# Kernel tuning notes

Measured on AMD Instinct MI355X. Metric: run time of the kernel, lower is better.

The kernel has to match this reference:

```python
import jax, jax.numpy as jnp
import numpy as np

B, T, D, H = 2, 2048, 1024, 16
DH = D // H
PD = 6
SCALE = DH ** -0.5
_PAIRS4 = [(0, 1), (0, 2), (0, 3), (1, 2), (1, 3), (2, 3)]
_J6 = jnp.array([[0, 0, 0, 0, 0, 1], [0, 0, 0, 0, -1, 0], [0, 0, 0, 1, 0, 0],
                 [0, 0, 1, 0, 0, 0], [0, -1, 0, 0, 0, 0], [1, 0, 0, 0, 0, 0]], dtype=jnp.float32)


def exterior(p1, p2):
    # p1, p2: (..., 4) -> normalized 6-d Plucker line (..., 6)
    parts = [p1[..., i] * p2[..., j] - p1[..., j] * p2[..., i] for i, j in _PAIRS4]
    L = jnp.stack(parts, axis=-1)
    n = jnp.linalg.norm(L, axis=-1, keepdims=True)
    return L / jnp.clip(n, 1e-12)


def setup_inputs() -> dict:
    key = jax.random.key(0)
    ks = jax.random.split(key, 12)
    s = 0.02
    return {
        'x': jax.random.normal(ks[0], (B, T, D), jnp.float32),
        'qkv_w': jax.random.normal(ks[1], (D, 3 * D), jnp.float32) * s,
        'qkv_b': jnp.zeros((3 * D,), jnp.float32),
        'w1_write': jax.random.normal(ks[2], (D, 4 * H), jnp.float32) * s,
        'w2_write': jax.random.normal(ks[3], (D, 4 * H), jnp.float32) * s,
        'w1_read': jax.random.normal(ks[4], (D, 4 * H), jnp.float32) * s,
        'w2_read': jax.random.normal(ks[5], (D, 4 * H), jnp.float32) * s,
        'memv_w': jax.random.normal(ks[6], (D, D), jnp.float32) * s,
        'memv_b': jnp.zeros((D,), jnp.float32),
        'memg_w': jax.random.normal(ks[7], (D, H), jnp.float32) * s,
        'memg_b': jnp.zeros((H,), jnp.float32),
        'mem_scale': jnp.full((H,), 0.1, jnp.float32),
        'rw_mix': jnp.zeros((), jnp.float32),
        'out_w': jax.random.normal(ks[8], (D, D), jnp.float32) * s,
        'out_b': jnp.zeros((D,), jnp.float32),
        'decay_logits': jnp.full((H,), 4.6, jnp.float32),
    }


def reference(x, qkv_w, qkv_b, w1_write, w2_write, w1_read, w2_read,
              memv_w, memv_b, memg_w, memg_b, mem_scale, rw_mix,
              out_w, out_b, decay_logits):
    # ---- standard causal softmax attention ----
    qkv = (x @ qkv_w + qkv_b).reshape(B, T, 3, H, DH).transpose(2, 0, 3, 1, 4)
    q, k, v = qkv[0], qkv[1], qkv[2]                      # each (B,H,T,DH)
    scores = jnp.einsum('bhtd,bhsd->bhts', q, k) * SCALE
    mask = jnp.triu(jnp.ones((T, T), bool), 1)
    scores = jnp.where(mask[None, None], -jnp.inf, scores)
    attn = jax.nn.softmax(scores, axis=-1)                # dropout=0 (eval)
    seq_out = jnp.einsum('bhts,bhsd->bthd', attn, v).reshape(B, T, D)

    # ---- Plucker lines for write (prev->cur) and read ----
    x_prev = jnp.concatenate([jnp.zeros((B, 1, D), x.dtype), x[:, :-1]], axis=1)
    w1 = (x_prev @ w1_write).reshape(B, T, H, 4)
    w2 = (x @ w2_write).reshape(B, T, H, 4)
    write_lines = exterior(w1, w2)                        # (B,T,H,6)
    r1 = (x @ w1_read).reshape(B, T, H, 4)
    r2 = (x @ w2_read).reshape(B, T, H, 4)
    read_lines = exterior(r1, r2)

    Jw = jnp.einsum('bthi,ij->bhtj', write_lines, _J6)    # (B,H,T,6)
    Jr = jnp.einsum('bthi,ij->bhtj', read_lines, _J6)
    rd = read_lines.transpose(0, 2, 1, 3)                 # (B,H,T,6)

    # ---- decay-weighted cumsum of 6x6 outer-product states ----
    decays = jax.nn.sigmoid(decay_logits)                 # (H,)
    pos = jnp.arange(T, dtype=x.dtype)
    decay_inv = (1.0 / jnp.clip(decays, 1e-6))[:, None] ** pos[None]   # (H,T)
    decay_fwd = decays[:, None] ** pos[None]                           # (H,T)

    def shifted_state(Jv):
        outer = Jv[..., :, None] * Jv[..., None, :]       # (B,H,T,6,6)
        ow = outer * decay_inv[None, :, :, None, None]
        M = jnp.cumsum(ow, axis=2)
        M = jnp.concatenate([jnp.zeros((B, H, 1, PD, PD), x.dtype), M[:, :, :-1]], axis=2)
        return M * decay_fwd[None, :, :, None, None]

    Mw = shifted_state(Jw)
    Mr = shifted_state(Jr)

    score_w = jnp.einsum('bhti,bhtij,bhtj->bht', rd, Mw, rd)
    score_r = jnp.einsum('bhti,bhtij,bhtj->bht', Jw, Mr, Jw)
    alpha = jax.nn.sigmoid(rw_mix)
    mem_score = (1 - alpha) * score_w + alpha * score_r   # (B,H,T)

    mem_val = x @ memv_w + memv_b                         # (B,T,D)
    gate = jax.nn.sigmoid(x @ memg_w + memg_b)            # (B,T,H)
    mem_score_t = mem_score.transpose(0, 2, 1)            # (B,T,H)
    gated = jax.nn.sigmoid(mem_score_t * mem_scale[None, None, :]) * gate
    gated = gated.mean(axis=-1, keepdims=True)            # (B,T,1)

    return (seq_out + gated * mem_val) @ out_w + out_b
```

## Files before the change

kernel.cpp:

```cpp
#include <hip/hip_runtime.h>

#define Bb 2
#define Tt 2048
#define Dd 1024
#define Hh 16
#define LDC 4480

typedef __attribute__((ext_vector_type(8))) short s16x8;
typedef __attribute__((ext_vector_type(4))) float f32x4;
typedef __attribute__((ext_vector_type(8))) _Float16 f16x8;

__device__ __forceinline__ float bf2f(unsigned short u) {
  unsigned v = ((unsigned)u) << 16;
  union { unsigned u; float f; } c; c.u = v; return c.f;
}
__device__ __forceinline__ unsigned short f2bf(float f) {
  union { float f; unsigned u; } c; c.f = f;
  unsigned u = c.u + 0x7fffu + ((c.u >> 16) & 1u);
  return (unsigned short)(u >> 16);
}
__device__ __forceinline__ float sigm(float x) { return 1.f / (1.f + expf(-x)); }

__device__ __forceinline__ int swz(int row, int k) {
  return (k & ~31) | (k & 7) | (((((k >> 3) & 3) ^ ((row >> 1) & 3))) << 3);
}

__device__ __forceinline__ void async_copy16(void* lds, const void* g) {
  __builtin_amdgcn_global_load_lds(
      (const __attribute__((address_space(1))) unsigned int*)g,
      (__attribute__((address_space(3))) unsigned int*)lds, 16, 0, 0);
}


__global__ __launch_bounds__(256) void prep_kernel(const float* __restrict__ x,
                                                   const float* __restrict__ qkv_w,
                                                   const float* __restrict__ w1w,
                                                   const float* __restrict__ w2w,
                                                   const float* __restrict__ w1r,
                                                   const float* __restrict__ w2r,
                                                   const float* __restrict__ memg_w,
                                                   const float* __restrict__ memv_w,
                                                   const float* __restrict__ out_w,
                                                   const float* __restrict__ qkv_b,
                                                   const float* __restrict__ memg_b,
                                                   const float* __restrict__ memv_b,
                                                   unsigned short* __restrict__ xb,
                                                   unsigned short* __restrict__ WT,
                                                   unsigned short* __restrict__ outT,
                                                   float* __restrict__ biasC) {
  __shared__ float tile[32][33];
  int id = blockIdx.x;
  if (id < 2048) {
    int i = id * 256 + threadIdx.x;
    int row = i >> 7;
    int colbase = (i & 127) * 8;
    const float4* xv = reinterpret_cast<const float4*>(x + (size_t)i * 8);
    float4 a = xv[0], b = xv[1];
    s16x8 out;
    out[0] = (short)f2bf(a.x); out[1] = (short)f2bf(a.y);
    out[2] = (short)f2bf(a.z); out[3] = (short)f2bf(a.w);
    out[4] = (short)f2bf(b.x); out[5] = (short)f2bf(b.y);
    out[6] = (short)f2bf(b.z); out[7] = (short)f2bf(b.w);
    *(s16x8*)&xb[(size_t)row * 1024 + swz(row, colbase)] = out;
  } else if (id < 6528) {
    int j = id - 2048;
    int n0 = (j % 140) * 32, k0 = (j / 140) * 32;
    int tx = threadIdx.x & 31, ty = threadIdx.x >> 5;
#pragma unroll
    for (int i = 0; i < 4; i++) {
      int k = k0 + ty + i * 8, n = n0 + tx;
      float v;
      if (n < 3072)       v = qkv_w[(size_t)k * 3072 + n];
      else if (n < 3136)  v = w1w[k * 64 + (n - 3072)];
      else if (n < 3200)  v = w2w[k * 64 + (n - 3136)];
      else if (n < 3264)  v = w1r[k * 64 + (n - 3200)];
      else if (n < 3328)  v = w2r[k * 64 + (n - 3264)];
      else if (n < 3344)  v = memg_w[k * 16 + (n - 3328)];
      else if (n < 3392)  v = 0.f;
      else if (n < 4416)  v = memv_w[(size_t)k * 1024 + (n - 3392)];
      else                v = 0.f;
      tile[ty + i * 8][tx] = v;
    }
    __syncthreads();
#pragma unroll
    for (int i = 0; i < 4; i++) {
      int n = n0 + ty + i * 8, k = k0 + tx;
      WT[(size_t)n * 1024 + swz(n, k)] = f2bf(tile[tx][ty + i * 8]);
    }
  } else if (id < 7552) {
    int j = id - 6528;
    int n0 = (j & 31) * 32, k0 = (j >> 5) * 32;
    int tx = threadIdx.x & 31, ty = threadIdx.x >> 5;
#pragma unroll
    for (int i = 0; i < 4; i++) {
      int k = k0 + ty + i * 8, n = n0 + tx;
      tile[ty + i * 8][tx] = out_w[(size_t)k * 1024 + n];
    }
    __syncthreads();
#pragma unroll
    for (int i = 0; i < 4; i++) {
      int n = n0 + ty + i * 8, k = k0 + tx;
      outT[(size_t)n * 1024 + swz(n, k)] = f2bf(tile[tx][ty + i * 8]);
    }
  } else {
    int i = (id - 7552) * 256 + threadIdx.x;
    if (i < LDC) {
      float v = 0.f;
      if (i < 3072) v = qkv_b[i];
      else if (i >= 3328 && i < 3344) v = memg_b[i - 3328];
      else if (i >= 3392 && i < 4416) v = memv_b[i - 3392];
      biasC[i] = v;
    }
  }
}


__global__ __launch_bounds__(256) void gemm_kernel(const unsigned short* __restrict__ A,
                                                   const unsigned short* __restrict__ Bt,
                                                   unsigned short* __restrict__ Cout,
                                                   const float* __restrict__ bias) {
  const int K = 1024;
  const int x = blockIdx.x & 7, local = blockIdx.x >> 3;
  const int mTile = (x >> 1) * 8 + (local & 7);
  const int nTile = (x & 1) * 18 + (local >> 3);
  if (nTile >= 35) return;
  const int mBase = mTile * 128, nBase = nTile * 128;

  __shared__ unsigned short As0[128 * 32], As1[128 * 32];
  __shared__ unsigned short Bs0[128 * 32], Bs1[128 * 32];
  const int tid = threadIdx.x;
  const int lane = tid & 63, wid = tid >> 6;
  const int quad = lane >> 4, c16 = lane & 15;
  const int wm = wid >> 1, wn = wid & 1;
  const int srow = lane >> 2, scol = (lane & 3) << 3;
  const int slot = (quad ^ ((c16 >> 1) & 3)) * 8;

  f32x4 acc[4][4] = {};
  for (int k0 = 0; k0 < K; k0 += 64) {
    __syncthreads();
#pragma unroll
    for (int j = 0; j < 2; j++) {
      int rr = wid * 32 + j * 16;
      size_t ga = (size_t)(mBase + rr + srow) * K + k0 + scol;
      size_t gb = (size_t)(nBase + rr + srow) * K + k0 + scol;
      async_copy16(&As0[rr * 32], &A[ga]);
      async_copy16(&Bs0[rr * 32], &Bt[gb]);
      async_copy16(&As1[rr * 32], &A[ga + 32]);
      async_copy16(&Bs1[rr * 32], &Bt[gb + 32]);
    }
    __syncthreads();
#pragma unroll
    for (int kk = 0; kk < 2; kk++) {
      const unsigned short* Asp = kk ? As1 : As0;
      const unsigned short* Bsp = kk ? Bs1 : Bs0;
      s16x8 af[4], bf[4];
#pragma unroll
      for (int mt = 0; mt < 4; mt++)
        af[mt] = *(const s16x8*)&Asp[(wm * 64 + mt * 16 + c16) * 32 + slot];
#pragma unroll
      for (int nt = 0; nt < 4; nt++)
        bf[nt] = *(const s16x8*)&Bsp[(wn * 64 + nt * 16 + c16) * 32 + slot];
#pragma unroll
      for (int mt = 0; mt < 4; mt++)
#pragma unroll
        for (int nt = 0; nt < 4; nt++)
          acc[mt][nt] = __builtin_amdgcn_mfma_f32_16x16x32_bf16(af[mt], bf[nt], acc[mt][nt], 0, 0, 0);
    }
  }
#pragma unroll
  for (int mt = 0; mt < 4; mt++)
#pragma unroll
    for (int nt = 0; nt < 4; nt++) {
      int col = nBase + wn * 64 + nt * 16 + c16;
      float bv = bias[col];
#pragma unroll
      for (int r = 0; r < 4; r++) {
        int row = mBase + wm * 64 + mt * 16 + quad * 4 + r;
        Cout[(size_t)row * 4480 + col] = f2bf(acc[mt][nt][r] + bv);
      }
    }
}


__global__ __launch_bounds__(256) void gemm_out_kernel(const unsigned short* __restrict__ A,
                                                       const unsigned short* __restrict__ Bt,
                                                       float* __restrict__ Cout,
                                                       const float* __restrict__ bias) {
  const int K = 1024;
  const int mBase = blockIdx.y * 64, nBase = blockIdx.x * 128;
  __shared__ unsigned short As0[64 * 32], As1[64 * 32];
  __shared__ unsigned short Bs0[128 * 32], Bs1[128 * 32];
  const int tid = threadIdx.x;
  const int lane = tid & 63, wid = tid >> 6;
  const int quad = lane >> 4, c16 = lane & 15;
  const int wm = wid >> 1, wn = wid & 1;
  const int srow = lane >> 2, scol = (lane & 3) << 3;
  const int slot = (quad ^ ((c16 >> 1) & 3)) * 8;

  f32x4 acc[2][4] = {};
  for (int k0 = 0; k0 < K; k0 += 64) {
    __syncthreads();
    {
      int rrA = wid * 16;
      size_t ga = (size_t)(mBase + rrA + srow) * K + k0 + scol;
      async_copy16(&As0[rrA * 32], &A[ga]);
      async_copy16(&As1[rrA * 32], &A[ga + 32]);
#pragma unroll
      for (int j = 0; j < 2; j++) {
        int rr = wid * 32 + j * 16;
        size_t gb = (size_t)(nBase + rr + srow) * K + k0 + scol;
        async_copy16(&Bs0[rr * 32], &Bt[gb]);
        async_copy16(&Bs1[rr * 32], &Bt[gb + 32]);
      }
    }
    __syncthreads();
#pragma unroll
    for (int kk = 0; kk < 2; kk++) {
      const unsigned short* Asp = kk ? As1 : As0;
      const unsigned short* Bsp = kk ? Bs1 : Bs0;
      s16x8 af[2], bf[4];
#pragma unroll
      for (int mt = 0; mt < 2; mt++)
        af[mt] = *(const s16x8*)&Asp[(wm * 32 + mt * 16 + c16) * 32 + slot];
#pragma unroll
      for (int nt = 0; nt < 4; nt++)
        bf[nt] = *(const s16x8*)&Bsp[(wn * 64 + nt * 16 + c16) * 32 + slot];
#pragma unroll
      for (int mt = 0; mt < 2; mt++)
#pragma unroll
        for (int nt = 0; nt < 4; nt++)
          acc[mt][nt] = __builtin_amdgcn_mfma_f32_16x16x32_bf16(af[mt], bf[nt], acc[mt][nt], 0, 0, 0);
    }
  }
#pragma unroll
  for (int mt = 0; mt < 2; mt++)
#pragma unroll
    for (int nt = 0; nt < 4; nt++) {
      int col = nBase + wn * 64 + nt * 16 + c16;
      float bv = bias[col];
#pragma unroll
      for (int r = 0; r < 4; r++) {
        int row = mBase + wm * 32 + mt * 16 + quad * 4 + r;
        Cout[(size_t)row * 1024 + col] = acc[mt][nt][r] + bv;
      }
    }
}


__device__ __forceinline__ void ext6(const float* p, const float* q, float* L) {
  L[0] = p[0] * q[1] - p[1] * q[0];
  L[1] = p[0] * q[2] - p[2] * q[0];
  L[2] = p[0] * q[3] - p[3] * q[0];
  L[3] = p[1] * q[2] - p[2] * q[1];
  L[4] = p[1] * q[3] - p[3] * q[1];
  L[5] = p[2] * q[3] - p[3] * q[2];
  float n = sqrtf(L[0]*L[0] + L[1]*L[1] + L[2]*L[2] + L[3]*L[3] + L[4]*L[4] + L[5]*L[5]);
  float inv = 1.f / fmaxf(n, 1e-12f);
#pragma unroll
  for (int k = 0; k < 6; k++) L[k] *= inv;
}


__global__ __launch_bounds__(256) void post1_kernel(const unsigned short* __restrict__ Cq,
                                                    unsigned short* __restrict__ Kt,
                                                    unsigned short* __restrict__ Vt,
                                                    float* __restrict__ Jw,
                                                    float* __restrict__ Jr,
                                                    float* __restrict__ rd) {
  __shared__ unsigned short vt[32 * 66];
  int id = blockIdx.x;
  int tid = threadIdx.x;
  if (id < 2048) {
    int kb = id & 63, bh = id >> 6;
    int b = bh >> 4, h = bh & 15;
    size_t tbase = ((size_t)bh * 64 + kb) * 2048;
    {
      int key = tid >> 3, p = tid & 7, dg = p ^ (key & 7);
      size_t src = (size_t)(b * Tt + kb * 32 + key) * LDC + 1024 + h * 64 + dg * 8;
      s16x8 kv = *(const s16x8*)&Cq[src];
      *(s16x8*)&Kt[tbase + (size_t)tid * 8] = kv;
    }
    {
      int row = tid >> 3, c = tid & 7;
      size_t src = (size_t)(b * Tt + kb * 32 + row) * LDC + 2048 + h * 64 + c * 8;
      s16x8 vv = *(const s16x8*)&Cq[src];
#pragma unroll
      for (int e = 0; e < 8; e++) {
        union { _Float16 hf; unsigned short s; } cv;
        cv.hf = (_Float16)bf2f((unsigned short)vv[e]);
        vt[row * 66 + c * 8 + e] = cv.s;
      }
    }
    __syncthreads();
    {
      int d = tid >> 2, p = tid & 3, cq = p ^ ((d >> 2) & 3);
      s16x8 out;
#pragma unroll
      for (int e = 0; e < 8; e++) {
        int key = ((e >> 2) & 1) * 16 + cq * 4 + (e & 3);
        out[e] = (short)vt[key * 66 + d];
      }
      *(s16x8*)&Vt[tbase + (size_t)tid * 8] = out;
    }
  } else {
    int idx = (id - 2048) * 256 + tid;
    int h = idx & 15, t = (idx >> 4) & 2047, b = idx >> 15;
    size_t row = (size_t)(b * Tt + t) * LDC;
    float w1[4], w2[4], r1[4], r2[4];
#pragma unroll
    for (int k = 0; k < 4; k++) {
      w1[k] = (t > 0) ? bf2f(Cq[row - LDC + 3072 + h * 4 + k]) : 0.f;
      w2[k] = bf2f(Cq[row + 3136 + h * 4 + k]);
      r1[k] = bf2f(Cq[row + 3200 + h * 4 + k]);
      r2[k] = bf2f(Cq[row + 3264 + h * 4 + k]);
    }
    float Lw[6], Lr[6];
    ext6(w1, w2, Lw);
    ext6(r1, r2, Lr);
    size_t ob = ((size_t)(b * Hh + h) * Tt + t) * 6;
    Jw[ob + 0] = Lw[5]; Jw[ob + 1] = -Lw[4]; Jw[ob + 2] = Lw[3];
    Jw[ob + 3] = Lw[2]; Jw[ob + 4] = -Lw[1]; Jw[ob + 5] = Lw[0];
    Jr[ob + 0] = Lr[5]; Jr[ob + 1] = -Lr[4]; Jr[ob + 2] = Lr[3];
    Jr[ob + 3] = Lr[2]; Jr[ob + 4] = -Lr[1]; Jr[ob + 5] = Lr[0];
#pragma unroll
    for (int k = 0; k < 6; k++) rd[ob + k] = Lr[k];
  }
}


__device__ __forceinline__ void do_tile(int ks, int q0, int quad, int c16,
                                        const s16x8& qf0, const s16x8& qf1,
                                        const s16x8 kf[2][2], const f16x8 vb[4],
                                        float& l_i, f32x4 o[4]) {
  f32x4 st0 = {}, st1 = {};
  st0 = __builtin_amdgcn_mfma_f32_16x16x32_bf16(kf[0][0], qf0, st0, 0, 0, 0);
  st0 = __builtin_amdgcn_mfma_f32_16x16x32_bf16(kf[0][1], qf1, st0, 0, 0, 0);
  st1 = __builtin_amdgcn_mfma_f32_16x16x32_bf16(kf[1][0], qf0, st1, 0, 0, 0);
  st1 = __builtin_amdgcn_mfma_f32_16x16x32_bf16(kf[1][1], qf1, st1, 0, 0, 0);
  bool need_mask = (ks + 31 > q0);
  f16x8 pa;
  float lp = 0.f;
#pragma unroll
  for (int r = 0; r < 4; r++) {
    float v0 = st0[r] * 0.125f;
    float v1 = st1[r] * 0.125f;
    if (need_mask) {
      v0 = (ks + quad * 4 + r      <= q0 + c16) ? v0 : -1e30f;
      v1 = (ks + 16 + quad * 4 + r <= q0 + c16) ? v1 : -1e30f;
    }
    float p0 = __expf(v0);
    float p1 = __expf(v1);
    lp += p0 + p1;
    pa[r]     = (_Float16)p0;
    pa[4 + r] = (_Float16)p1;
  }
  l_i += lp;
#pragma unroll
  for (int nt = 0; nt < 4; nt++)
    o[nt] = __builtin_amdgcn_mfma_f32_16x16x32_f16(pa, vb[nt], o[nt], 0, 0, 0);
}

__global__ __launch_bounds__(256) void attn_kernel(const unsigned short* __restrict__ Cq,
                                                   const unsigned short* __restrict__ Kt,
                                                   const unsigned short* __restrict__ Vt,
                                                   unsigned short* __restrict__ po) {
  __shared__ unsigned short Kl[2048];
  __shared__ unsigned short Vl[2048];
  const int g0 = blockIdx.x, bh = blockIdx.y;
  const int g = ((bh >> 4) & 1) ? (15 - g0) : g0;
  const int b = bh >> 4, h = bh & 15;
  const int w = threadIdx.x >> 6, lane = threadIdx.x & 63;
  const int quad = lane >> 4, c16 = lane & 15;
  const int pi = g * 4 + w;
  const int qA = pi * 16, qB = 2032 - pi * 16;
  const int nkA = qA + 16, nkB = 2048 - pi * 16;
  const int bound = 2048 - 64 * g;
  const unsigned short* Ktb = Kt + (size_t)bh * 64 * 2048;
  const unsigned short* Vtb = Vt + (size_t)bh * 64 * 2048;
  const int ci = threadIdx.x;

  size_t rowA = (size_t)(b * Tt + qA + c16) * LDC + h * 64;
  size_t rowB = (size_t)(b * Tt + qB + c16) * LDC + h * 64;
  s16x8 qA0 = *(const s16x8*)&Cq[rowA + quad * 8];
  s16x8 qA1 = *(const s16x8*)&Cq[rowA + 32 + quad * 8];
  s16x8 qB0 = *(const s16x8*)&Cq[rowB + quad * 8];
  s16x8 qB1 = *(const s16x8*)&Cq[rowB + 32 + quad * 8];

  float lA = 0.f, lB = 0.f;
  f32x4 oA[4] = {}, oB[4] = {};

  {
    s16x8 k0 = *(const s16x8*)&Ktb[(size_t)ci * 8];
    s16x8 v0 = *(const s16x8*)&Vtb[(size_t)ci * 8];
    *(s16x8*)&Kl[ci * 8] = k0;
    *(s16x8*)&Vl[ci * 8] = v0;
  }
  __syncthreads();

  for (int ks = 0; ks < bound; ks += 32) {
    bool more = (ks + 32) < bound;
    s16x8 kreg, vreg;
    if (more) {
      size_t nb = ((size_t)(ks >> 5) + 1) * 2048 + (size_t)ci * 8;
      kreg = *(const s16x8*)&Ktb[nb];
      vreg = *(const s16x8*)&Vtb[nb];
    }
    if (ks < nkB) {
      s16x8 kf[2][2];
#pragma unroll
      for (int gg = 0; gg < 2; gg++)
#pragma unroll
        for (int half = 0; half < 2; half++) {
          int key = gg * 16 + c16;
          int p = (half * 4 + quad) ^ (c16 & 7);
          kf[gg][half] = *(const s16x8*)&Kl[(key * 8 + p) * 8];
        }
      f16x8 vb[4];
#pragma unroll
      for (int nt = 0; nt < 4; nt++) {
        int d = nt * 16 + c16;
        int p = quad ^ ((d >> 2) & 3);
        vb[nt] = *(const f16x8*)&Vl[(d * 4 + p) * 8];
      }
      do_tile(ks, qB, quad, c16, qB0, qB1, kf, vb, lB, oB);
      if (ks < nkA)
        do_tile(ks, qA, quad, c16, qA0, qA1, kf, vb, lA, oA);
    }
    __syncthreads();
    if (more) {
      *(s16x8*)&Kl[ci * 8] = kreg;
      *(s16x8*)&Vl[ci * 8] = vreg;
      __syncthreads();
    }
  }

  lB += __shfl_xor(lB, 16, 64); lB += __shfl_xor(lB, 32, 64);
  lA += __shfl_xor(lA, 16, 64); lA += __shfl_xor(lA, 32, 64);
  float invB = 1.f / lB, invA = 1.f / lA;
#pragma unroll
  for (int r = 0; r < 4; r++) {
    float ivB = __shfl(invB, quad * 4 + r, 64);
    float ivA = __shfl(invA, quad * 4 + r, 64);
    size_t baseB = (size_t)(b * Tt + qB + quad * 4 + r) * Dd + h * 64;
    size_t baseA = (size_t)(b * Tt + qA + quad * 4 + r) * Dd + h * 64;
#pragma unroll
    for (int nt = 0; nt < 4; nt++) {
      po[baseB + nt * 16 + c16] = f2bf(oB[nt][r] * ivB);
      po[baseA + nt * 16 + c16] = f2bf(oA[nt][r] * ivA);
    }
  }
}


__global__ __launch_bounds__(64) void scanA_kernel(const float* __restrict__ Jw,
                                                   const float* __restrict__ Jr,
                                                   const float* __restrict__ decay_logits,
                                                   float* __restrict__ chunkA) {
  int blk = blockIdx.x;
  int chunk = blk & 15, bh = (blk >> 4) & 31, type = blk >> 9;
  int lane = threadIdx.x;
  const float* V = (type == 0 ? Jw : Jr) + ((size_t)bh * Tt + chunk * 128) * 6;
  __shared__ float v[768];
  for (int i = lane; i < 768; i += 64) v[i] = V[i];
  __syncthreads();
  float d = sigm(decay_logits[bh & 15]);
  int ll = lane < 36 ? lane : 35;
  int i6 = ll / 6, j6 = ll % 6;
  float A = 0.f;
  for (int s = 0; s < 128; s++) A = d * A + v[s * 6 + i6] * v[s * 6 + j6];
  if (lane < 36) chunkA[((size_t)(type * 32 + bh) * 16 + chunk) * 36 + lane] = A;
}


__global__ __launch_bounds__(128) void scanB_kernel(const float* __restrict__ Jw,
                                                    const float* __restrict__ Jr,
                                                    const float* __restrict__ rd,
                                                    const float* __restrict__ chunkA,
                                                    const float* __restrict__ decay_logits,
                                                    float* __restrict__ score_w,
                                                    float* __restrict__ score_r) {
  int blk = blockIdx.x;
  int chunk = blk & 15, bh = (blk >> 4) & 31, type = blk >> 9;
  int tl = threadIdx.x;
  size_t tb = ((size_t)bh * Tt + chunk * 128) * 6;
  const float* U = (type == 0 ? rd : Jw) + tb;
  const float* W = (type == 0 ? Jw : Jr) + tb;
  __shared__ float wv[768];
  __shared__ float Bm[36];
  for (int i = tl; i < 768; i += 128) wv[i] = W[i];
  float d = sigm(decay_logits[bh & 15]);
  if (tl < 36) {
    float dS = powf(d, 128.f);
    float Bv = 0.f;
    size_t base = (size_t)(type * 32 + bh) * 16;
    for (int c = 0; c < chunk; c++)
      Bv = dS * Bv + d * chunkA[(base + c) * 36 + tl];
    Bm[tl] = Bv;
  }
  __syncthreads();
  float u[6];
#pragma unroll
  for (int i = 0; i < 6; i++) u[i] = U[tl * 6 + i];
  float q = 0.f;
#pragma unroll
  for (int i = 0; i < 6; i++) {
    float bi = 0.f;
#pragma unroll
    for (int j = 0; j < 6; j++) bi += Bm[i * 6 + j] * u[j];
    q += u[i] * bi;
  }
  float acc = 0.f;
  for (int s = 0; s < tl; s++) {
    const float* ws = &wv[s * 6];
    float dot = u[0]*ws[0] + u[1]*ws[1] + u[2]*ws[2] + u[3]*ws[3] + u[4]*ws[4] + u[5]*ws[5];
    acc = d * (acc + dot * dot);
  }
  float score = acc + powf(d, (float)tl) * q;
  float* outp = (type == 0 ? score_w : score_r);
  outp[(size_t)bh * Tt + chunk * 128 + tl] = score;
}


__global__ __launch_bounds__(256) void combine_kernel(const unsigned short* __restrict__ po,
                                                      const unsigned short* __restrict__ Cq,
                                                      const float* __restrict__ score_w,
                                                      const float* __restrict__ score_r,
                                                      const float* __restrict__ mem_scale,
                                                      const float* __restrict__ rw_mix,
                                                      unsigned short* __restrict__ fused) {
  __shared__ float tmp[16];
  int rowi = blockIdx.x;
  int b = rowi >> 11, t = rowi & 2047;
  float alpha = sigm(rw_mix[0]);
  if (threadIdx.x < 16) {
    int h = threadIdx.x;
    size_t sh = (size_t)(b * 16 + h) * Tt + t;
    float ms = (1.f - alpha) * score_w[sh] + alpha * score_r[sh];
    float gate = sigm(bf2f(Cq[(size_t)rowi * LDC + 3328 + h]));
    tmp[h] = sigm(ms * mem_scale[h]) * gate;
  }
  __syncthreads();
  float g = 0.f;
#pragma unroll
  for (int h = 0; h < 16; h++) g += tmp[h];
  g *= (1.f / 16.f);
  for (int d = threadIdx.x; d < Dd; d += 256) {
    float sv = bf2f(po[((size_t)b * Tt + t) * Dd + d]);
    float mv = bf2f(Cq[(size_t)rowi * LDC + 3392 + d]);
    fused[(size_t)rowi * Dd + swz(rowi, d)] = f2bf(sv + g * mv);
  }
}


extern "C" void kernel_launch(void* const* d_in, const int* in_sizes, int n_in,
                              void* d_out, int out_size, void* d_ws, size_t ws_size,
                              hipStream_t stream) {
  (void)in_sizes; (void)n_in; (void)out_size; (void)ws_size;
  const float* x         = (const float*)d_in[0];
  const float* qkv_w     = (const float*)d_in[1];
  const float* qkv_b     = (const float*)d_in[2];
  const float* w1w       = (const float*)d_in[3];
  const float* w2w       = (const float*)d_in[4];
  const float* w1r       = (const float*)d_in[5];
  const float* w2r       = (const float*)d_in[6];
  const float* memv_w    = (const float*)d_in[7];
  const float* memv_b    = (const float*)d_in[8];
  const float* memg_w    = (const float*)d_in[9];
  const float* memg_b    = (const float*)d_in[10];
  const float* mem_scale = (const float*)d_in[11];
  const float* rw_mix    = (const float*)d_in[12];
  const float* out_w     = (const float*)d_in[13];
  const float* out_b     = (const float*)d_in[14];
  const float* decay_l   = (const float*)d_in[15];

  char* w = (char*)d_ws;
  unsigned short* xb    = (unsigned short*)(w + 0);
  unsigned short* Kt    = (unsigned short*)(w + 0);
  unsigned short* WT    = (unsigned short*)(w + 8388608);
  unsigned short* Vt    = (unsigned short*)(w + 8388608);
  unsigned short* outT  = (unsigned short*)(w + 17563648);
  float*          biasC = (float*)(w + 19660800);
  unsigned short* Cbuf  = (unsigned short*)(w + 19678720);
  unsigned short* po    = (unsigned short*)(w + 56378880);
  float*          Jw    = (float*)(w + 73680384);
  float*          Jr    = (float*)(w + 75253248);
  float*          rd    = (float*)(w + 76826112);
  float*          chA   = (float*)(w + 78398976);
  float*          sw    = (float*)(w + 78693888);
  float*          sr    = (float*)(w + 78956032);
  unsigned short* fused = (unsigned short*)(w + 79218176);

  prep_kernel<<<7570, 256, 0, stream>>>(x, qkv_w, w1w, w2w, w1r, w2r, memg_w, memv_w,
                                        out_w, qkv_b, memg_b, memv_b,
                                        xb, WT, outT, biasC);

  gemm_kernel<<<1152, 256, 0, stream>>>(xb, WT, Cbuf, biasC);

  post1_kernel<<<2304, 256, 0, stream>>>(Cbuf, Kt, Vt, Jw, Jr, rd);
  attn_kernel<<<dim3(16, 32), 256, 0, stream>>>(Cbuf, Kt, Vt, po);
  scanA_kernel<<<1024, 64, 0, stream>>>(Jw, Jr, decay_l, chA);
  scanB_kernel<<<1024, 128, 0, stream>>>(Jw, Jr, rd, chA, decay_l, sw, sr);
  combine_kernel<<<4096, 256, 0, stream>>>(po, Cbuf, sw, sr, mem_scale, rw_mix, fused);

  gemm_out_kernel<<<dim3(8, 64), 256, 0, stream>>>(fused, outT, (float*)d_out, out_b);
}
```

Baseline: 283.8 us.

## Pre-pack GEMM operands in MFMA fragment order and load straight to registers

The prep and combine kernels now write the x, weight and fused activation matrices in a 16-row-tile, MFMA-fragment-native order, so each lane's 8-element fragment is one contiguous 16-byte load. Both GEMMs are replaced by one templated kernel that reads fragments directly from global memory into double-buffered registers, with no LDS staging and no barriers. The output GEMM also moves from 64x128 to 128x128 tiles. The aim is to remove LDS traffic and synchronisation overhead. In exchange, waves sharing a tile reload the same operands through cache, and the single-step register prefetch may not hide global load latency.

```diff
diff --git a/kernel.cpp b/kernel.cpp
--- a/kernel.cpp
+++ b/kernel.cpp
@@ -21,15 +21,6 @@
 }
 __device__ __forceinline__ float sigm(float x) { return 1.f / (1.f + expf(-x)); }
 
-__device__ __forceinline__ int swz(int row, int k) {
-  return (k & ~31) | (k & 7) | (((((k >> 3) & 3) ^ ((row >> 1) & 3))) << 3);
-}
-
-__device__ __forceinline__ void async_copy16(void* lds, const void* g) {
-  __builtin_amdgcn_global_load_lds(
-      (const __attribute__((address_space(1))) unsigned int*)g,
-      (__attribute__((address_space(3))) unsigned int*)lds, 16, 0, 0);
-}
 
 
 __global__ __launch_bounds__(256) void prep_kernel(const float* __restrict__ x,
@@ -53,7 +44,7 @@
   if (id < 2048) {
     int i = id * 256 + threadIdx.x;
     int row = i >> 7;
-    int colbase = (i & 127) * 8;
+    int k8 = i & 127;
     const float4* xv = reinterpret_cast<const float4*>(x + (size_t)i * 8);
     float4 a = xv[0], b = xv[1];
     s16x8 out;
@@ -61,10 +52,12 @@
     out[2] = (short)f2bf(a.z); out[3] = (short)f2bf(a.w);
     out[4] = (short)f2bf(b.x); out[5] = (short)f2bf(b.y);
     out[6] = (short)f2bf(b.z); out[7] = (short)f2bf(b.w);
-    *(s16x8*)&xb[(size_t)row * 1024 + swz(row, colbase)] = out;
+    int mt = row >> 4, kt = k8 >> 2, quad = k8 & 3;
+    int lane = (row & 15) + quad * 16;
+    *(s16x8*)&xb[(((size_t)mt * 32 + kt) * 64 + lane) * 8] = out;
   } else if (id < 6528) {
     int j = id - 2048;
-    int n0 = (j % 140) * 32, k0 = (j / 140) * 32;
+    int n0 = (j % 140) * 32, kt = j / 140, k0 = kt * 32;
     int tx = threadIdx.x & 31, ty = threadIdx.x >> 5;
 #pragma unroll
     for (int i = 0; i < 4; i++) {
@@ -82,14 +75,18 @@
       tile[ty + i * 8][tx] = v;
     }
     __syncthreads();
-#pragma unroll
-    for (int i = 0; i < 4; i++) {
-      int n = n0 + ty + i * 8, k = k0 + tx;
-      WT[(size_t)n * 1024 + swz(n, k)] = f2bf(tile[tx][ty + i * 8]);
+    if (threadIdx.x < 128) {
+      int nl = threadIdx.x & 31, quad = threadIdx.x >> 5;
+      s16x8 out;
+#pragma unroll
+      for (int e = 0; e < 8; e++) out[e] = (short)f2bf(tile[quad * 8 + e][nl]);
+      int nt = (n0 >> 4) + (nl >> 4);
+      int lane = (nl & 15) + quad * 16;
+      *(s16x8*)&WT[(((size_t)nt * 32 + kt) * 64 + lane) * 8] = out;
     }
   } else if (id < 7552) {
     int j = id - 6528;
-    int n0 = (j & 31) * 32, k0 = (j >> 5) * 32;
+    int n0 = (j & 31) * 32, kt = j >> 5, k0 = kt * 32;
     int tx = threadIdx.x & 31, ty = threadIdx.x >> 5;
 #pragma unroll
     for (int i = 0; i < 4; i++) {
@@ -97,10 +94,14 @@
       tile[ty + i * 8][tx] = out_w[(size_t)k * 1024 + n];
     }
     __syncthreads();
-#pragma unroll
-    for (int i = 0; i < 4; i++) {
-      int n = n0 + ty + i * 8, k = k0 + tx;
-      outT[(size_t)n * 1024 + swz(n, k)] = f2bf(tile[tx][ty + i * 8]);
+    if (threadIdx.x < 128) {
+      int nl = threadIdx.x & 31, quad = threadIdx.x >> 5;
+      s16x8 out;
+#pragma unroll
+      for (int e = 0; e < 8; e++) out[e] = (short)f2bf(tile[quad * 8 + e][nl]);
+      int nt = (n0 >> 4) + (nl >> 4);
+      int lane = (nl & 15) + quad * 16;
+      *(s16x8*)&outT[(((size_t)nt * 32 + kt) * 64 + lane) * 8] = out;
     }
   } else {
     int i = (id - 7552) * 256 + threadIdx.x;
@@ -115,133 +116,69 @@
 }
 
 
-__global__ __launch_bounds__(256) void gemm_kernel(const unsigned short* __restrict__ A,
-                                                   const unsigned short* __restrict__ Bt,
-                                                   unsigned short* __restrict__ Cout,
-                                                   const float* __restrict__ bias) {
-  const int K = 1024;
-  const int x = blockIdx.x & 7, local = blockIdx.x >> 3;
-  const int mTile = (x >> 1) * 8 + (local & 7);
-  const int nTile = (x & 1) * 18 + (local >> 3);
-  if (nTile >= 35) return;
-  const int mBase = mTile * 128, nBase = nTile * 128;
-
-  __shared__ unsigned short As0[128 * 32], As1[128 * 32];
-  __shared__ unsigned short Bs0[128 * 32], Bs1[128 * 32];
-  const int tid = threadIdx.x;
-  const int lane = tid & 63, wid = tid >> 6;
+template <int MODE>
+__global__ __launch_bounds__(256) void gemm_frag_kernel(const unsigned short* __restrict__ Af,
+                                                        const unsigned short* __restrict__ Bf,
+                                                        void* __restrict__ Cout,
+                                                        const float* __restrict__ bias) {
+  int mTile, nTile;
+  if (MODE == 0) {
+    const int xx = blockIdx.x & 7, local = blockIdx.x >> 3;
+    mTile = (xx >> 1) * 8 + (local & 7);
+    nTile = (xx & 1) * 18 + (local >> 3);
+    if (nTile >= 35) return;
+  } else {
+    mTile = blockIdx.x >> 3;
+    nTile = blockIdx.x & 7;
+  }
+  const int lane = threadIdx.x & 63, wid = threadIdx.x >> 6;
   const int quad = lane >> 4, c16 = lane & 15;
   const int wm = wid >> 1, wn = wid & 1;
-  const int srow = lane >> 2, scol = (lane & 3) << 3;
-  const int slot = (quad ^ ((c16 >> 1) & 3)) * 8;
+  const int mt0 = mTile * 8 + wm * 4;
+  const int nt0 = nTile * 8 + wn * 4;
+  const unsigned short* Apt = Af + ((size_t)mt0 * 32 * 64 + lane) * 8;
+  const unsigned short* Bpt = Bf + ((size_t)nt0 * 32 * 64 + lane) * 8;
 
   f32x4 acc[4][4] = {};
-  for (int k0 = 0; k0 < K; k0 += 64) {
-    __syncthreads();
-#pragma unroll
-    for (int j = 0; j < 2; j++) {
-      int rr = wid * 32 + j * 16;
-      size_t ga = (size_t)(mBase + rr + srow) * K + k0 + scol;
-      size_t gb = (size_t)(nBase + rr + srow) * K + k0 + scol;
-      async_copy16(&As0[rr * 32], &A[ga]);
-      async_copy16(&Bs0[rr * 32], &Bt[gb]);
-      async_copy16(&As1[rr * 32], &A[ga + 32]);
-      async_copy16(&Bs1[rr * 32], &Bt[gb + 32]);
-    }
-    __syncthreads();
-#pragma unroll
-    for (int kk = 0; kk < 2; kk++) {
-      const unsigned short* Asp = kk ? As1 : As0;
-      const unsigned short* Bsp = kk ? Bs1 : Bs0;
-      s16x8 af[4], bf[4];
-#pragma unroll
-      for (int mt = 0; mt < 4; mt++)
-        af[mt] = *(const s16x8*)&Asp[(wm * 64 + mt * 16 + c16) * 32 + slot];
+  s16x8 af[2][4], bf[2][4];
+#pragma unroll
+  for (int i = 0; i < 4; i++) {
+    af[0][i] = *(const s16x8*)(Apt + (size_t)i * 16384);
+    bf[0][i] = *(const s16x8*)(Bpt + (size_t)i * 16384);
+  }
+#pragma unroll
+  for (int kt = 0; kt < 32; kt++) {
+    const int cur = kt & 1, nxt = cur ^ 1;
+    if (kt + 1 < 32) {
+      const unsigned short* An = Apt + (size_t)(kt + 1) * 512;
+      const unsigned short* Bn = Bpt + (size_t)(kt + 1) * 512;
+#pragma unroll
+      for (int i = 0; i < 4; i++) {
+        af[nxt][i] = *(const s16x8*)(An + (size_t)i * 16384);
+        bf[nxt][i] = *(const s16x8*)(Bn + (size_t)i * 16384);
+      }
+    }
+#pragma unroll
+    for (int mt = 0; mt < 4; mt++)
 #pragma unroll
       for (int nt = 0; nt < 4; nt++)
-        bf[nt] = *(const s16x8*)&Bsp[(wn * 64 + nt * 16 + c16) * 32 + slot];
-#pragma unroll
-      for (int mt = 0; mt < 4; mt++)
-#pragma unroll
-        for (int nt = 0; nt < 4; nt++)
-          acc[mt][nt] = __builtin_amdgcn_mfma_f32_16x16x32_bf16(af[mt], bf[nt], acc[mt][nt], 0, 0, 0);
-    }
-  }
+        acc[mt][nt] = __builtin_amdgcn_mfma_f32_16x16x32_bf16(af[cur][mt], bf[cur][nt],
+                                                              acc[mt][nt], 0, 0, 0);
+  }
+
 #pragma unroll
   for (int mt = 0; mt < 4; mt++)
 #pragma unroll
     for (int nt = 0; nt < 4; nt++) {
-      int col = nBase + wn * 64 + nt * 16 + c16;
+      int col = (nt0 + nt) * 16 + c16;
       float bv = bias[col];
 #pragma unroll
       for (int r = 0; r < 4; r++) {
-        int row = mBase + wm * 64 + mt * 16 + quad * 4 + r;
-        Cout[(size_t)row * 4480 + col] = f2bf(acc[mt][nt][r] + bv);
-      }
-    }
-}
-
-
-__global__ __launch_bounds__(256) void gemm_out_kernel(const unsigned short* __restrict__ A,
-                                                       const unsigned short* __restrict__ Bt,
-                                                       float* __restrict__ Cout,
-                                                       const float* __restrict__ bias) {
-  const int K = 1024;
-  const int mBase = blockIdx.y * 64, nBase = blockIdx.x * 128;
-  __shared__ unsigned short As0[64 * 32], As1[64 * 32];
-  __shared__ unsigned short Bs0[128 * 32], Bs1[128 * 32];
-  const int tid = threadIdx.x;
-  const int lane = tid & 63, wid = tid >> 6;
-  const int quad = lane >> 4, c16 = lane & 15;
-  const int wm = wid >> 1, wn = wid & 1;
-  const int srow = lane >> 2, scol = (lane & 3) << 3;
-  const int slot = (quad ^ ((c16 >> 1) & 3)) * 8;
-
-  f32x4 acc[2][4] = {};
-  for (int k0 = 0; k0 < K; k0 += 64) {
-    __syncthreads();
-    {
-      int rrA = wid * 16;
-      size_t ga = (size_t)(mBase + rrA + srow) * K + k0 + scol;
-      async_copy16(&As0[rrA * 32], &A[ga]);
-      async_copy16(&As1[rrA * 32], &A[ga + 32]);
-#pragma unroll
-      for (int j = 0; j < 2; j++) {
-        int rr = wid * 32 + j * 16;
-        size_t gb = (size_t)(nBase + rr + srow) * K + k0 + scol;
-        async_copy16(&Bs0[rr * 32], &Bt[gb]);
-        async_copy16(&Bs1[rr * 32], &Bt[gb + 32]);
-      }
-    }
-    __syncthreads();
-#pragma unroll
-    for (int kk = 0; kk < 2; kk++) {
-      const unsigned short* Asp = kk ? As1 : As0;
-      const unsigned short* Bsp = kk ? Bs1 : Bs0;
-      s16x8 af[2], bf[4];
-#pragma unroll
-      for (int mt = 0; mt < 2; mt++)
-        af[mt] = *(const s16x8*)&Asp[(wm * 32 + mt * 16 + c16) * 32 + slot];
-#pragma unroll
-      for (int nt = 0; nt < 4; nt++)
-        bf[nt] = *(const s16x8*)&Bsp[(wn * 64 + nt * 16 + c16) * 32 + slot];
-#pragma unroll
-      for (int mt = 0; mt < 2; mt++)
-#pragma unroll
-        for (int nt = 0; nt < 4; nt++)
-          acc[mt][nt] = __builtin_amdgcn_mfma_f32_16x16x32_bf16(af[mt], bf[nt], acc[mt][nt], 0, 0, 0);
-    }
-  }
-#pragma unroll
-  for (int mt = 0; mt < 2; mt++)
-#pragma unroll
-    for (int nt = 0; nt < 4; nt++) {
-      int col = nBase + wn * 64 + nt * 16 + c16;
-      float bv = bias[col];
-#pragma unroll
-      for (int r = 0; r < 4; r++) {
-        int row = mBase + wm * 32 + mt * 16 + quad * 4 + r;
-        Cout[(size_t)row * 1024 + col] = acc[mt][nt][r] + bv;
+        int row = (mt0 + mt) * 16 + quad * 4 + r;
+        if (MODE == 0)
+          ((unsigned short*)Cout)[(size_t)row * 4480 + col] = f2bf(acc[mt][nt][r] + bv);
+        else
+          ((float*)Cout)[(size_t)row * 1024 + col] = acc[mt][nt][r] + bv;
       }
     }
 }
@@ -544,10 +481,18 @@
 #pragma unroll
   for (int h = 0; h < 16; h++) g += tmp[h];
   g *= (1.f / 16.f);
-  for (int d = threadIdx.x; d < Dd; d += 256) {
-    float sv = bf2f(po[((size_t)b * Tt + t) * Dd + d]);
-    float mv = bf2f(Cq[(size_t)rowi * LDC + 3392 + d]);
-    fused[(size_t)rowi * Dd + swz(rowi, d)] = f2bf(sv + g * mv);
+  if (threadIdx.x < 128) {
+    int c = threadIdx.x;
+    int d0 = c * 8;
+    s16x8 ov = *(const s16x8*)&po[((size_t)b * Tt + t) * Dd + d0];
+    s16x8 mv = *(const s16x8*)&Cq[(size_t)rowi * LDC + 3392 + d0];
+    s16x8 out;
+#pragma unroll
+    for (int e = 0; e < 8; e++)
+      out[e] = (short)f2bf(bf2f((unsigned short)ov[e]) + g * bf2f((unsigned short)mv[e]));
+    int mt = rowi >> 4, kt = c >> 2, quad = c & 3;
+    int lane = (rowi & 15) + quad * 16;
+    *(s16x8*)&fused[(((size_t)mt * 32 + kt) * 64 + lane) * 8] = out;
   }
 }
 
@@ -594,7 +539,7 @@
                                         out_w, qkv_b, memg_b, memv_b,
                                         xb, WT, outT, biasC);
 
-  gemm_kernel<<<1152, 256, 0, stream>>>(xb, WT, Cbuf, biasC);
+  gemm_frag_kernel<0><<<1152, 256, 0, stream>>>(xb, WT, Cbuf, biasC);
 
   post1_kernel<<<2304, 256, 0, stream>>>(Cbuf, Kt, Vt, Jw, Jr, rd);
   attn_kernel<<<dim3(16, 32), 256, 0, stream>>>(Cbuf, Kt, Vt, po);
@@ -602,5 +547,5 @@
   scanB_kernel<<<1024, 128, 0, stream>>>(Jw, Jr, rd, chA, decay_l, sw, sr);
   combine_kernel<<<4096, 256, 0, stream>>>(po, Cbuf, sw, sr, mem_scale, rw_mix, fused);
 
-  gemm_out_kernel<<<dim3(8, 64), 256, 0, stream>>>(fused, outT, (float*)d_out, out_b);
-}
+  gemm_frag_kernel<1><<<256, 256, 0, stream>>>(fused, outT, d_out, out_b);
+}
```

Result: no change. 278.3 us (-1.9%).
